# Optimization experiments

Measured on AMD Instinct MI355X. Metric: run time of the kernel, lower is better.

Reference implementation:

```python
import jax, jax.numpy as jnp
import numpy as np

THRESH = 0.59275  # PercolationQ default threshold
SIZES = list(range(3, 42, 2))  # 20 Chebyshev scales
B, P, C = 16, 100, 3


def _connected_components(imgs):
    # imgs: (N, s, s) int32 in {0,1}. 4-connectivity CC via min-label propagation.
    # Label value = (min flat index in component) + 1, background = 0.
    N, s, _ = imgs.shape
    big = s * s + 1
    fg = imgs > 0
    idx = jnp.arange(s * s, dtype=jnp.int32).reshape(1, s, s) + 1
    init = jnp.where(fg, idx, big)

    def body(state):
        L, _ = state
        Lp = jnp.pad(L, ((0, 0), (1, 1), (1, 1)), constant_values=big)
        m = jnp.minimum(jnp.minimum(Lp[:, :-2, 1:-1], Lp[:, 2:, 1:-1]),
                        jnp.minimum(Lp[:, 1:-1, :-2], Lp[:, 1:-1, 2:]))
        Ln = jnp.where(fg, jnp.minimum(L, m), big)
        return Ln, jnp.any(Ln != L)

    L, _ = jax.lax.while_loop(lambda st: st[1], body, (init, jnp.bool_(True)))
    return jnp.where(fg, L, 0)


def _scale_features(x):
    b, p, s, _, c = x.shape
    # --- Chebyshev layer (faithful to the TF reshape + center-crop semantics) ---
    r = x.reshape(b * s, p, s, c)
    center = r[:, (p - 1) // 2, (s - 1) // 2, :][:, None, None, :]
    binm = (jnp.abs(r - center).max(axis=3) <= float(s)).astype(jnp.int32).reshape(b, p, s, s)
    # --- Probability: histogram of per-patch foreground counts ---
    counts = binm.sum(axis=(2, 3))  # (b, p), values in [0, s^2]
    L = s * s + 1
    hist = jax.vmap(lambda cc: jnp.bincount(cc, length=L))(counts).astype(jnp.float32) / p
    numbers = jnp.concatenate([jnp.ones((1,), jnp.float32), jnp.arange(1, L, dtype=jnp.float32)])
    # --- FractalDimension / Lacunarity ---
    fd = (hist / numbers).sum(axis=1)
    mu1 = (hist * numbers).sum(axis=1) ** 2
    mu2 = (hist * numbers ** 2).sum(axis=1)
    lac = (mu2 - mu1) / mu1
    # --- PercolationQ ---
    pq = ((counts.astype(jnp.float32) / (s * s)) >= THRESH).astype(jnp.float32).mean(axis=1)
    # --- Clusterize (tfa semantics: labels unique/consecutive across the whole batch) ---
    labels = _connected_components(binm.reshape(b * p, s, s))
    lhist = jax.vmap(lambda l: jnp.bincount(l.ravel(), length=L))(labels)  # (b*p, s^2+1)
    ncomp = (lhist[:, 1:] > 0).sum(axis=1)
    # max global label in image i = cumulative component count (0 if no components)
    maxlab = jnp.where(ncomp > 0, jnp.cumsum(ncomp), 0)
    pc = maxlab.astype(jnp.float32).reshape(b, p).mean(axis=1)
    # PercolationM: max bincount over per-sample flattened global labels
    #   = max(total background pixels, largest component size in the sample)
    bg = lhist[:, 0].reshape(b, p).sum(axis=1)
    maxcomp = lhist[:, 1:].max(axis=1).reshape(b, p).max(axis=1)
    pm = jnp.maximum(bg, maxcomp).astype(jnp.float32)
    return fd, lac, pq, pc, pm


def _forward(xs):
    feats = [_scale_features(x) for x in xs]
    fd = jnp.stack([f[0] for f in feats], axis=1)
    lac = jnp.stack([f[1] for f in feats], axis=1)
    pq = jnp.stack([f[2] for f in feats], axis=1)
    pc = jnp.stack([f[3] for f in feats], axis=1)
    pm = jnp.stack([f[4] for f in feats], axis=1)
    out = jnp.concatenate([pc, pq, pm, lac, fd], axis=1)  # (B, 100)
    return out.reshape(-1, 10, 10)


def setup_inputs() -> dict:
    key = jax.random.key(0)
    inp = {}
    for i, s in enumerate(SIZES):
        inp[f"x{i}"] = jax.random.normal(jax.random.fold_in(key, i), (B, P, s, s, C), dtype=jnp.float32)
    return inp


def reference(x0, x1, x2, x3, x4, x5, x6, x7, x8, x9, x10, x11, x12, x13, x14, x15, x16, x17, x18, x19):
    return _forward([x0, x1, x2, x3, x4, x5, x6, x7, x8, x9, x10, x11, x12, x13, x14, x15, x16, x17, x18, x19])
```

## Files before the change

### kernel.cpp

```cpp
#include <hip/hip_runtime.h>

#define NSCALES 20
#define PATCH 100
#define IMGS_PER_SCALE 1600
#define TOTAL_IMGS 32000
#define THREADS 256
#define CHUNKPX 2048
#define NF4BLK (CHUNKPX * 3 / 4)
#define F4PT (NF4BLK / THREADS)
#define MAXIMG 240
#define S2MAX 1681

struct Ptrs   { const float* p[NSCALES]; };
struct Starts { int blkStart[NSCALES]; };

template<int S>
__device__ __forceinline__ void count_body(const float* __restrict__ x,
                                           int blkLocal, int sc,
                                           int* __restrict__ wsC2,
                                           float4* stgF4, float4* cenL,
                                           int* cntL)
{
    constexpr int S2 = S * S;
    constexpr int ROWDIV = 100 * S;
    const int Ntot   = IMGS_PER_SCALE * S2;
    const int NF4tot = Ntot * 3 / 4;
    const int P0     = blkLocal * CHUNKPX;
    const int Pend   = min(P0 + CHUNKPX, Ntot);
    const int tid    = threadIdx.x;

    const int imgBase = P0 / S2;
    const int imgLast = (Pend - 1) / S2;
    const int nImg    = imgLast - imgBase + 1;
    const int j0      = P0 / ROWDIV;
    const int jEnd    = (Pend - 1) / ROWDIV;
    const int nj      = jEnd - j0 + 1;

    const float4* __restrict__ x4 = (const float4*)x;
    const int F0 = blkLocal * NF4BLK;
    float4 stg[F4PT];
    #pragma unroll
    for (int it = 0; it < F4PT; it++) {
        int fi = F0 + it * THREADS + tid;
        stg[it] = x4[min(fi, NF4tot - 1)];
    }
    if (tid < nj) {
        int j = j0 + tid;
        const float* c = x + (size_t)(((j * PATCH + 49) * S + (S >> 1)) * 3);
        cenL[tid] = make_float4(c[0], c[1], c[2], 0.f);
    }
    for (int t = tid; t < nImg; t += THREADS) cntL[t] = 0;
    #pragma unroll
    for (int it = 0; it < F4PT; it++) stgF4[it * THREADS + tid] = stg[it];
    __syncthreads();

    const float* lf = (const float*)stgF4;
    #pragma unroll
    for (int half = 0; half < 2; half++) {
        const int p0 = P0 + half * (CHUNKPX / 2) + tid * 4;
        if (p0 < Pend) {
            const float4* src = (const float4*)(lf + (size_t)(p0 - P0) * 3);
            float4 a = src[0], b = src[1], c = src[2];
            const float f[12] = {a.x,a.y,a.z,a.w, b.x,b.y,b.z,b.w,
                                 c.x,c.y,c.z,c.w};
            const int iA = p0 / S2;
            const int r0 = p0 - iA * S2;
            const int jA = p0 / ROWDIV;
            const int jB = (p0 + 3) / ROWDIV;
            const float4 ceA = cenL[jA - j0];
            const float4 ceB = (jB != jA) ? cenL[jB - j0] : ceA;
            const int flip = (jB != jA) ? ((jA + 1) * ROWDIV - p0) : 4;

            int cA = 0, cB = 0;
            #pragma unroll
            for (int q = 0; q < 4; q++) {
                const float4 ce = (q < flip) ? ceA : ceB;
                float d = fmaxf(fmaxf(fabsf(f[q*3+0] - ce.x),
                                      fabsf(f[q*3+1] - ce.y)),
                                fabsf(f[q*3+2] - ce.z));
                int fg = (d <= (float)S) ? 1 : 0;
                int t  = r0 + q;
                cA += (t < S2) ? fg : 0;
                cB += (t >= S2) ? fg : 0;
            }
            atomicAdd(&cntL[iA - imgBase], cA);
            if (cB) atomicAdd(&cntL[iA + 1 - imgBase], cB);
        }
    }
    __syncthreads();

    for (int t = tid; t < nImg; t += THREADS) {
        int img = imgBase + t;
        int lo = img * S2, hi = lo + S2;
        int g = sc * IMGS_PER_SCALE + img;
        int vv = cntL[t];
        if (lo >= P0) {
            wsC2[2 * g] = vv;
            if (hi <= Pend) wsC2[2 * g + 1] = 0;
        } else {
            wsC2[2 * g + 1] = vv;
        }
    }
}

__global__ __launch_bounds__(THREADS)
void count_kernel(Ptrs ptrs, Starts st, int* __restrict__ wsC2)
{
    const int bid = blockIdx.x;
    int sc = 0;
    #pragma unroll
    for (int k = 1; k < NSCALES; k++) sc += (bid >= st.blkStart[k]) ? 1 : 0;
    const int blkLocal = bid - st.blkStart[sc];

    __shared__ float4 stgF4[NF4BLK];
    __shared__ float4 cenL[8];
    __shared__ int    cntL[MAXIMG];

    switch (sc) {
#define CASE(i) case i: count_body<3 + 2*(i)>(ptrs.p[i], blkLocal, i, wsC2, stgF4, cenL, cntL); break;
        CASE(0)  CASE(1)  CASE(2)  CASE(3)  CASE(4)
        CASE(5)  CASE(6)  CASE(7)  CASE(8)  CASE(9)
        CASE(10) CASE(11) CASE(12) CASE(13) CASE(14)
        CASE(15) CASE(16) CASE(17) CASE(18) CASE(19)
#undef CASE
    }
}

__global__ __launch_bounds__(THREADS)
void cc_kernel(Ptrs ptrs, const int* __restrict__ wsC2,
               int* __restrict__ wsCnt,
               int* __restrict__ wsNcomp, int* __restrict__ wsMaxc)
{
    const int bid = blockIdx.x;
    const int sc  = bid / 25;
    const int s   = 3 + 2 * sc;
    const int s2  = s * s;
    const int BIGL = s2 + 1;
    const float* __restrict__ x = ptrs.p[sc];
    const int imgLoc0 = (bid % 25) * 64;
    const int tid = threadIdx.x;
    const unsigned mS = 0xFFFFFFFFu / (unsigned)s + 1;

    __shared__ int slowList[64];
    __shared__ int nslow;
    __shared__ int lab[S2MAX];
    __shared__ int szh[S2MAX];
    __shared__ int redN[4], redM[4];

    if (tid == 0) nslow = 0;
    __syncthreads();
    if (tid < 64) {
        int img = imgLoc0 + tid;
        int g = sc * IMGS_PER_SCALE + img;
        int c = wsC2[2 * g] + wsC2[2 * g + 1];
        wsCnt[g] = c;
        if (c == s2)      { wsNcomp[g] = 1; wsMaxc[g] = s2; }
        else if (c == 0)  { wsNcomp[g] = 0; wsMaxc[g] = 0; }
        else { int k = atomicAdd(&nslow, 1); slowList[k] = img; }
    }
    __syncthreads();
    const int ns = nslow;
    if (ns == 0) return;

    if (s2 <= 64) {
        const int w = tid >> 6, l = tid & 63;
        for (int idx = w; idx < ns; idx += 4) {
            int img = slowList[idx];
            int fg = 0, labr = BIGL, i1 = 0, i2 = 0;
            if (l < s2) {
                i1 = (int)__umulhi((unsigned)l, mS);
                i2 = l - i1 * s;
                int M = img * s + i1;
                int j = M / PATCH;
                const float* ce = x + (size_t)(((j * PATCH + 49) * s + (s >> 1)) * 3);
                const float* px = x + ((size_t)img * s2 + l) * 3;
                float d = fmaxf(fmaxf(fabsf(px[0] - ce[0]), fabsf(px[1] - ce[1])),
                                fabsf(px[2] - ce[2]));
                if (d <= (float)s) { fg = 1; labr = l + 1; }
            }
            for (;;) {
                int m = labr;
                int vU = __shfl(labr, (l - s) & 63);
                int vD = __shfl(labr, (l + s) & 63);
                int vL = __shfl(labr, (l - 1) & 63);
                int vR = __shfl(labr, (l + 1) & 63);
                if (fg) {
                    if (i1 > 0)     m = min(m, vU);
                    if (i1 < s - 1) m = min(m, vD);
                    if (i2 > 0)     m = min(m, vL);
                    if (i2 < s - 1) m = min(m, vR);
                }
                int vJ = __shfl(labr, (m - 1) & 63);
                if (fg) m = min(m, vJ);
                unsigned long long chg = __ballot(m < labr);
                labr = m;
                if (chg == 0) break;
            }
            int ncomp = __popcll(__ballot(fg && labr == l + 1));
            int mc = 0;
            for (int r = 0; r < s2; r++) {
                int szr = __popcll(__ballot(fg && labr == r + 1));
                mc = max(mc, szr);
            }
            if (l == 0) {
                int g = sc * IMGS_PER_SCALE + img;
                wsNcomp[g] = ncomp; wsMaxc[g] = mc;
            }
        }
    } else {
        for (int idx = 0; idx < ns; idx++) {
            int img = slowList[idx];
            const int ibase = img * s2 * 3;
            for (int i = tid; i < s2; i += THREADS) {
                int i1 = (int)__umulhi((unsigned)i, mS);
                int M = img * s + i1;
                int j = M / PATCH;
                const float* ce = x + (size_t)(((j * PATCH + 49) * s + (s >> 1)) * 3);
                const float* px = x + ibase + i * 3;
                float d = fmaxf(fmaxf(fabsf(px[0] - ce[0]), fabsf(px[1] - ce[1])),
                                fabsf(px[2] - ce[2]));
                lab[i] = (d <= (float)s) ? (i + 1) : BIGL;
                szh[i] = 0;
            }
            __syncthreads();
            for (;;) {
                bool changed = false;
                for (int i = tid; i < s2; i += THREADS) {
                    int L0 = lab[i];
                    if (L0 <= s2) {
                        int i1 = (int)__umulhi((unsigned)i, mS);
                        int i2 = i - i1 * s;
                        int m = L0;
                        if (i1 > 0)     m = min(m, lab[i - s]);
                        if (i1 < s - 1) m = min(m, lab[i + s]);
                        if (i2 > 0)     m = min(m, lab[i - 1]);
                        if (i2 < s - 1) m = min(m, lab[i + 1]);
                        m = min(m, lab[m - 1]);
                        if (m < L0) { lab[i] = m; changed = true; }
                    }
                }
                if (__syncthreads_count(changed ? 1 : 0) == 0) break;
            }
            int ncomp = 0;
            for (int i = tid; i < s2; i += THREADS) {
                int L = lab[i];
                if (L <= s2) {
                    atomicAdd(&szh[L - 1], 1);
                    if (L == i + 1) ncomp++;
                }
            }
            __syncthreads();
            int mc = 0;
            for (int i = tid; i < s2; i += THREADS) mc = max(mc, szh[i]);
            for (int m = 32; m >= 1; m >>= 1) {
                ncomp += __shfl_xor(ncomp, m);
                mc     = max(mc, __shfl_xor(mc, m));
            }
            int wid = tid >> 6, lane = tid & 63;
            if (lane == 0) { redN[wid] = ncomp; redM[wid] = mc; }
            __syncthreads();
            if (tid == 0) {
                int g = sc * IMGS_PER_SCALE + img;
                wsNcomp[g] = redN[0] + redN[1] + redN[2] + redN[3];
                wsMaxc[g]  = max(max(redM[0], redM[1]), max(redM[2], redM[3]));
            }
            __syncthreads();
        }
    }
}

__global__ __launch_bounds__(THREADS)
void final_kernel(const int* __restrict__ wsCnt,
                  const int* __restrict__ wsNcomp,
                  const int* __restrict__ wsMaxc,
                  float* __restrict__ out)
{
    const int scale = blockIdx.x;
    const int s  = 3 + 2 * scale;
    const int s2 = s * s;
    const int tid = threadIdx.x;
    const int NB = IMGS_PER_SCALE;
    const int CH = 7;

    __shared__ int nc[IMGS_PER_SCALE];
    __shared__ int tsum[THREADS];

    for (int i = tid; i < NB; i += THREADS) nc[i] = wsNcomp[scale * NB + i];
    __syncthreads();

    int lsum = 0;
    for (int k = 0; k < CH; k++) {
        int idx = tid * CH + k;
        if (idx < NB) lsum += nc[idx];
    }
    tsum[tid] = lsum;
    __syncthreads();
    for (int st = 1; st < THREADS; st <<= 1) {
        int v = (tid >= st) ? tsum[tid - st] : 0;
        __syncthreads();
        tsum[tid] += v;
        __syncthreads();
    }
    int run = (tid > 0) ? tsum[tid - 1] : 0;
    for (int k = 0; k < CH; k++) {
        int idx = tid * CH + k;
        if (idx < NB) {
            int v = nc[idx];
            run += v;
            nc[idx] = (v > 0) ? run : 0;
        }
    }
    __syncthreads();

    int b    = tid >> 4;
    int lane = tid & 15;
    float fdsum = 0.f, sn = 0.f, sn2 = 0.f, pcsum = 0.f;
    int pqc = 0, bg = 0, mcx = 0;
    for (int q = lane; q < PATCH; q += 16) {
        int i = b * PATCH + q;
        int c = wsCnt[scale * NB + i];
        float n = (c > 0) ? (float)c : 1.0f;
        fdsum += 1.0f / n;
        sn    += n;
        sn2   += n * n;
        pqc   += ((float)c / (float)s2 >= 0.59275f) ? 1 : 0;
        bg    += (s2 - c);
        mcx    = max(mcx, wsMaxc[scale * NB + i]);
        pcsum += (float)nc[i];
    }
    for (int m = 8; m >= 1; m >>= 1) {
        fdsum += __shfl_xor(fdsum, m);
        sn    += __shfl_xor(sn, m);
        sn2   += __shfl_xor(sn2, m);
        pcsum += __shfl_xor(pcsum, m);
        pqc   += __shfl_xor(pqc, m);
        bg    += __shfl_xor(bg, m);
        mcx    = max(mcx, __shfl_xor(mcx, m));
    }
    if (lane == 0) {
        float fd  = fdsum / 100.0f;
        float m1  = sn / 100.0f;
        float mu1 = m1 * m1;
        float mu2 = sn2 / 100.0f;
        float lac = (mu2 - mu1) / mu1;
        float pq  = (float)pqc / 100.0f;
        float pc  = pcsum / 100.0f;
        float pm  = (float)max(bg, mcx);
        out[b * 100 +  0 + scale] = pc;
        out[b * 100 + 20 + scale] = pq;
        out[b * 100 + 40 + scale] = pm;
        out[b * 100 + 60 + scale] = lac;
        out[b * 100 + 80 + scale] = fd;
    }
}

extern "C" void kernel_launch(void* const* d_in, const int* in_sizes, int n_in,
                              void* d_out, int out_size, void* d_ws, size_t ws_size,
                              hipStream_t stream)
{
    Ptrs ptrs;
    for (int i = 0; i < NSCALES; i++) ptrs.p[i] = (const float*)d_in[i];

    Starts st;
    int acc = 0;
    for (int i = 0; i < NSCALES; i++) {
        st.blkStart[i] = acc;
        int s = 3 + 2 * i, s2 = s * s;
        acc += (IMGS_PER_SCALE * s2 + CHUNKPX - 1) / CHUNKPX;
    }

    int* wsC2  = (int*)d_ws;
    int* wsCnt = wsC2 + 2 * TOTAL_IMGS;
    int* wsN   = wsCnt + TOTAL_IMGS;
    int* wsM   = wsN + TOTAL_IMGS;

    count_kernel<<<acc, THREADS, 0, stream>>>(ptrs, st, wsC2);
    cc_kernel<<<TOTAL_IMGS / 64, THREADS, 0, stream>>>(ptrs, wsC2, wsCnt, wsN, wsM);
    final_kernel<<<NSCALES, THREADS, 0, stream>>>(wsCnt, wsN, wsM, (float*)d_out);
}
```

Before: 67.63 us.

## Make count kernel persistent with register double-buffered prefetch and slotted counters

Turns the count kernel into a persistent grid of fixed size that walks chunks in a strided loop and prefetches the next chunk's data into registers while the current one is computed. Each thread now loads contiguous float4s straight into registers instead of staging them through shared memory, and patch centers are read from global memory per thread. Per-image shared counters are split into four slots to reduce atomic contention. This aims to hide global load latency and cut shared-memory traffic, at the cost of more registers, extra barriers per chunk and redundant center loads.

New measurement: 69.40 us. 1.03x slower.

```diff
diff --git a/kernel.cpp b/kernel.cpp
--- a/kernel.cpp
+++ b/kernel.cpp
@@ -6,99 +6,101 @@
 #define TOTAL_IMGS 32000
 #define THREADS 256
 #define CHUNKPX 2048
-#define NF4BLK (CHUNKPX * 3 / 4)
-#define F4PT (NF4BLK / THREADS)
-#define MAXIMG 240
+#define NF4CHUNK 1536
+#define NBLK 2560
+#define SLOTS 4
+#define CNTSZ 1024
 #define S2MAX 1681
 
 struct Ptrs   { const float* p[NSCALES]; };
-struct Starts { int blkStart[NSCALES]; };
+struct Starts { int chunkStart[NSCALES]; int nchunks; };
+
+__device__ __forceinline__ void issue_loads(const float4* __restrict__ x4,
+                                            int FC, int NF4tot, int tid,
+                                            float4* v)
+{
+    #pragma unroll
+    for (int i = 0; i < 3; i++) v[i]     = x4[min(FC + tid * 3 + i, NF4tot - 1)];
+    #pragma unroll
+    for (int i = 0; i < 3; i++) v[3 + i] = x4[min(FC + 768 + tid * 3 + i, NF4tot - 1)];
+}
 
 template<int S>
-__device__ __forceinline__ void count_body(const float* __restrict__ x,
-                                           int blkLocal, int sc,
-                                           int* __restrict__ wsC2,
-                                           float4* stgF4, float4* cenL,
-                                           int* cntL)
+__device__ __forceinline__ void compute_chunk(const float* __restrict__ x,
+                                              int chunkLocal, const float4* v,
+                                              int tid, int* cntL)
 {
     constexpr int S2 = S * S;
     constexpr int ROWDIV = 100 * S;
-    const int Ntot   = IMGS_PER_SCALE * S2;
-    const int NF4tot = Ntot * 3 / 4;
-    const int P0     = blkLocal * CHUNKPX;
-    const int Pend   = min(P0 + CHUNKPX, Ntot);
-    const int tid    = threadIdx.x;
-
+    const int Ntot = IMGS_PER_SCALE * S2;
+    const int P0   = chunkLocal * CHUNKPX;
+    const int Pend = min(P0 + CHUNKPX, Ntot);
     const int imgBase = P0 / S2;
-    const int imgLast = (Pend - 1) / S2;
-    const int nImg    = imgLast - imgBase + 1;
-    const int j0      = P0 / ROWDIV;
-    const int jEnd    = (Pend - 1) / ROWDIV;
-    const int nj      = jEnd - j0 + 1;
-
-    const float4* __restrict__ x4 = (const float4*)x;
-    const int F0 = blkLocal * NF4BLK;
-    float4 stg[F4PT];
+    const int slot = tid & (SLOTS - 1);
+
     #pragma unroll
-    for (int it = 0; it < F4PT; it++) {
-        int fi = F0 + it * THREADS + tid;
-        stg[it] = x4[min(fi, NF4tot - 1)];
-    }
-    if (tid < nj) {
-        int j = j0 + tid;
-        const float* c = x + (size_t)(((j * PATCH + 49) * S + (S >> 1)) * 3);
-        cenL[tid] = make_float4(c[0], c[1], c[2], 0.f);
-    }
-    for (int t = tid; t < nImg; t += THREADS) cntL[t] = 0;
-    #pragma unroll
-    for (int it = 0; it < F4PT; it++) stgF4[it * THREADS + tid] = stg[it];
-    __syncthreads();
-
-    const float* lf = (const float*)stgF4;
-    #pragma unroll
-    for (int half = 0; half < 2; half++) {
-        const int p0 = P0 + half * (CHUNKPX / 2) + tid * 4;
+    for (int g = 0; g < 2; g++) {
+        const int p0 = P0 + g * (CHUNKPX / 2) + tid * 4;
         if (p0 < Pend) {
-            const float4* src = (const float4*)(lf + (size_t)(p0 - P0) * 3);
-            float4 a = src[0], b = src[1], c = src[2];
-            const float f[12] = {a.x,a.y,a.z,a.w, b.x,b.y,b.z,b.w,
-                                 c.x,c.y,c.z,c.w};
+            const float4 A = v[3 * g], B = v[3 * g + 1], C = v[3 * g + 2];
             const int iA = p0 / S2;
             const int r0 = p0 - iA * S2;
             const int jA = p0 / ROWDIV;
             const int jB = (p0 + 3) / ROWDIV;
-            const float4 ceA = cenL[jA - j0];
-            const float4 ceB = (jB != jA) ? cenL[jB - j0] : ceA;
-            const int flip = (jB != jA) ? ((jA + 1) * ROWDIV - p0) : 4;
-
+            const float* ceA = x + (size_t)(((jA * PATCH + 49) * S + (S >> 1)) * 3);
+            float a0 = ceA[0], a1 = ceA[1], a2 = ceA[2];
+            float b0 = a0, b1 = a1, b2 = a2;
+            int flip = 4;
+            if (jB != jA) {
+                const float* ceB = x + (size_t)(((jB * PATCH + 49) * S + (S >> 1)) * 3);
+                b0 = ceB[0]; b1 = ceB[1]; b2 = ceB[2];
+                flip = (jA + 1) * ROWDIV - p0;
+            }
             int cA = 0, cB = 0;
             #pragma unroll
             for (int q = 0; q < 4; q++) {
-                const float4 ce = (q < flip) ? ceA : ceB;
-                float d = fmaxf(fmaxf(fabsf(f[q*3+0] - ce.x),
-                                      fabsf(f[q*3+1] - ce.y)),
-                                fabsf(f[q*3+2] - ce.z));
+                float f0 = (q==0)?A.x:(q==1)?A.w:(q==2)?B.z:C.y;
+                float f1 = (q==0)?A.y:(q==1)?B.x:(q==2)?B.w:C.z;
+                float f2 = (q==0)?A.z:(q==1)?B.y:(q==2)?C.x:C.w;
+                float e0 = (q < flip) ? a0 : b0;
+                float e1 = (q < flip) ? a1 : b1;
+                float e2 = (q < flip) ? a2 : b2;
+                float d = fmaxf(fmaxf(fabsf(f0 - e0), fabsf(f1 - e1)),
+                                fabsf(f2 - e2));
                 int fg = (d <= (float)S) ? 1 : 0;
                 int t  = r0 + q;
                 cA += (t < S2) ? fg : 0;
                 cB += (t >= S2) ? fg : 0;
             }
-            atomicAdd(&cntL[iA - imgBase], cA);
-            if (cB) atomicAdd(&cntL[iA + 1 - imgBase], cB);
-        }
-    }
-    __syncthreads();
-
+            atomicAdd(&cntL[(iA - imgBase) * SLOTS + slot], cA);
+            if (cB) atomicAdd(&cntL[(iA + 1 - imgBase) * SLOTS + slot], cB);
+        }
+    }
+}
+
+template<int S>
+__device__ __forceinline__ void flush_chunk(int chunkLocal, int sc,
+                                            const int* cntL,
+                                            int* __restrict__ wsC2, int tid)
+{
+    constexpr int S2 = S * S;
+    const int Ntot = IMGS_PER_SCALE * S2;
+    const int P0   = chunkLocal * CHUNKPX;
+    const int Pend = min(P0 + CHUNKPX, Ntot);
+    const int imgBase = P0 / S2;
+    const int imgLast = (Pend - 1) / S2;
+    const int nImg = imgLast - imgBase + 1;
     for (int t = tid; t < nImg; t += THREADS) {
         int img = imgBase + t;
         int lo = img * S2, hi = lo + S2;
+        int v = cntL[t * SLOTS] + cntL[t * SLOTS + 1]
+              + cntL[t * SLOTS + 2] + cntL[t * SLOTS + 3];
         int g = sc * IMGS_PER_SCALE + img;
-        int vv = cntL[t];
         if (lo >= P0) {
-            wsC2[2 * g] = vv;
+            wsC2[2 * g] = v;
             if (hi <= Pend) wsC2[2 * g + 1] = 0;
         } else {
-            wsC2[2 * g + 1] = vv;
+            wsC2[2 * g + 1] = v;
         }
     }
 }
@@ -106,23 +108,54 @@
 __global__ __launch_bounds__(THREADS)
 void count_kernel(Ptrs ptrs, Starts st, int* __restrict__ wsC2)
 {
-    const int bid = blockIdx.x;
+    __shared__ int cntL[CNTSZ];
+    const int tid = threadIdx.x;
+    float4 vA[6], vB[6];
+
+    int c = blockIdx.x;
     int sc = 0;
     #pragma unroll
-    for (int k = 1; k < NSCALES; k++) sc += (bid >= st.blkStart[k]) ? 1 : 0;
-    const int blkLocal = bid - st.blkStart[sc];
-
-    __shared__ float4 stgF4[NF4BLK];
-    __shared__ float4 cenL[8];
-    __shared__ int    cntL[MAXIMG];
-
-    switch (sc) {
-#define CASE(i) case i: count_body<3 + 2*(i)>(ptrs.p[i], blkLocal, i, wsC2, stgF4, cenL, cntL); break;
-        CASE(0)  CASE(1)  CASE(2)  CASE(3)  CASE(4)
-        CASE(5)  CASE(6)  CASE(7)  CASE(8)  CASE(9)
-        CASE(10) CASE(11) CASE(12) CASE(13) CASE(14)
-        CASE(15) CASE(16) CASE(17) CASE(18) CASE(19)
+    for (int k = 1; k < NSCALES; k++) sc += (c >= st.chunkStart[k]) ? 1 : 0;
+    {
+        int cl = c - st.chunkStart[sc];
+        int s = 3 + 2 * sc;
+        int NF4 = IMGS_PER_SCALE * s * s * 3 / 4;
+        issue_loads((const float4*)ptrs.p[sc], cl * NF4CHUNK, NF4, tid, vA);
+    }
+    for (int t = tid; t < CNTSZ; t += THREADS) cntL[t] = 0;
+    __syncthreads();
+
+    for (;;) {
+        const int cn = c + NBLK;
+        int scn = 0;
+        if (cn < st.nchunks) {
+            #pragma unroll
+            for (int k = 1; k < NSCALES; k++) scn += (cn >= st.chunkStart[k]) ? 1 : 0;
+            int cln = cn - st.chunkStart[scn];
+            int s = 3 + 2 * scn;
+            int NF4 = IMGS_PER_SCALE * s * s * 3 / 4;
+            issue_loads((const float4*)ptrs.p[scn], cln * NF4CHUNK, NF4, tid, vB);
+        }
+
+        const int cl = c - st.chunkStart[sc];
+        switch (sc) {
+#define CASE(i) case i: \
+            compute_chunk<3 + 2*(i)>(ptrs.p[i], cl, vA, tid, cntL); \
+            __syncthreads(); \
+            flush_chunk<3 + 2*(i)>(cl, i, cntL, wsC2, tid); break;
+            CASE(0)  CASE(1)  CASE(2)  CASE(3)  CASE(4)
+            CASE(5)  CASE(6)  CASE(7)  CASE(8)  CASE(9)
+            CASE(10) CASE(11) CASE(12) CASE(13) CASE(14)
+            CASE(15) CASE(16) CASE(17) CASE(18) CASE(19)
 #undef CASE
+        }
+        __syncthreads();
+        for (int t = tid; t < CNTSZ; t += THREADS) cntL[t] = 0;
+        if (cn >= st.nchunks) break;
+        __syncthreads();
+        #pragma unroll
+        for (int i = 0; i < 6; i++) vA[i] = vB[i];
+        c = cn; sc = scn;
     }
 }
 
@@ -364,17 +397,18 @@
     Starts st;
     int acc = 0;
     for (int i = 0; i < NSCALES; i++) {
-        st.blkStart[i] = acc;
+        st.chunkStart[i] = acc;
         int s = 3 + 2 * i, s2 = s * s;
         acc += (IMGS_PER_SCALE * s2 + CHUNKPX - 1) / CHUNKPX;
     }
+    st.nchunks = acc;
 
     int* wsC2  = (int*)d_ws;
     int* wsCnt = wsC2 + 2 * TOTAL_IMGS;
     int* wsN   = wsCnt + TOTAL_IMGS;
     int* wsM   = wsN + TOTAL_IMGS;
 
-    count_kernel<<<acc, THREADS, 0, stream>>>(ptrs, st, wsC2);
+    count_kernel<<<NBLK, THREADS, 0, stream>>>(ptrs, st, wsC2);
     cc_kernel<<<TOTAL_IMGS / 64, THREADS, 0, stream>>>(ptrs, wsC2, wsCnt, wsN, wsM);
     final_kernel<<<NSCALES, THREADS, 0, stream>>>(wsCnt, wsN, wsM, (float*)d_out);
 }
```
